# Kernel optimization log

Measured on AMD Instinct MI355X. Metric: run time of the kernel, lower is better.

## Reference

```python
import jax, jax.numpy as jnp
import numpy as np

EPS = 1e-5  # BatchNorm eps; BN applied in eval mode with running_mean=0, running_var=1


def conv1x1(x, w, b=None):
    # x: [B,C,H,W], w: [O,C] -> [B,O,H,W]
    y = jnp.einsum('bchw,oc->bohw', x, w)
    if b is not None:
        y = y + b[None, :, None, None]
    return y


def bn_eval(x, gamma, beta):
    # running_mean=0, running_var=1
    scale = gamma / jnp.sqrt(1.0 + EPS)
    return x * scale[None, :, None, None] + beta[None, :, None, None]


def glnl_forward(x, mask, wt_nl, bt_nl, wp_nl, bp_nl, wt_l, bt_l, wp_l, bp_l,
                 wg_nl, bg_nl, wg_l, bg_l, wW, bW, gW, betaW, wWl, gWl, betaWl):
    B, C, H, W = x.shape
    I = wt_nl.shape[0]
    N = H * W

    # non-local branch score [B,N,N]
    th_nl = conv1x1(x, wt_nl, bt_nl).reshape(B, I, N)
    ph_nl = conv1x1(x, wp_nl, bp_nl).reshape(B, I, N)
    score_nl = jax.nn.softmax(jnp.einsum('bin,bim->bnm', th_nl, ph_nl), axis=-1)

    # local branch: mask-gated projections, score [B,N,N]
    m = mask.reshape(B, 1, N)
    th_l = conv1x1(x, wt_l, bt_l).reshape(B, I, N) * m
    ph_l = conv1x1(x, wp_l, bp_l).reshape(B, I, N) * m
    score_l = jax.nn.softmax(jnp.einsum('bin,bim->bnm', th_l, ph_l), axis=-1)

    # value projections [B,I,N]
    g_nl = conv1x1(x, wg_nl, bg_nl).reshape(B, I, N)
    g_l = conv1x1(x, wg_l, bg_l).reshape(B, I, N)

    # attention aggregation -> [B,I,H,W]
    y_nl = jnp.einsum('bnm,bim->bin', score_nl, g_nl).reshape(B, I, H, W)
    y_l = jnp.einsum('bnm,bim->bin', score_l, g_l).reshape(B, I, H, W)

    # W_local: conv1x1 (no bias) -> ReLU -> BN
    y_l = bn_eval(jax.nn.relu(conv1x1(y_l, wWl)), gWl, betaWl)

    y = y_nl + y_l
    # W: conv1x1 -> ReLU -> BN, then residual
    W_y = bn_eval(jax.nn.relu(conv1x1(y, wW, bW)), gW, betaW)
    return W_y + x


def setup_inputs() -> dict:
    key = jax.random.key(0)
    ks = jax.random.split(key, 20)
    B, C, I, H, W = 4, 128, 64, 64, 64
    s = 0.02
    inp = {
        'x': jax.random.normal(ks[0], (B, C, H, W), jnp.float32),
        'mask': (jax.random.uniform(ks[1], (B, 1, H, W)) > 0.5).astype(jnp.float32),
        'wt_nl': jax.random.normal(ks[2], (I, C)) * s, 'bt_nl': jnp.zeros((I,)),
        'wp_nl': jax.random.normal(ks[3], (I, C)) * s, 'bp_nl': jnp.zeros((I,)),
        'wt_l': jax.random.normal(ks[4], (I, C)) * s, 'bt_l': jnp.zeros((I,)),
        'wp_l': jax.random.normal(ks[5], (I, C)) * s, 'bp_l': jnp.zeros((I,)),
        'wg_nl': jax.random.normal(ks[6], (I, C)) * s, 'bg_nl': jnp.zeros((I,)),
        'wg_l': jax.random.normal(ks[7], (I, C)) * s, 'bg_l': jnp.zeros((I,)),
        'wW': jax.random.normal(ks[8], (C, I)) * s, 'bW': jnp.zeros((C,)),
        'gW': jnp.ones((C,)), 'betaW': jnp.zeros((C,)),
        'wWl': jax.random.normal(ks[9], (I, I)) * s,
        'gWl': jnp.ones((I,)), 'betaWl': jnp.zeros((I,)),
    }
    return inp


def reference(x, mask, wt_nl, bt_nl, wp_nl, bp_nl, wt_l, bt_l, wp_l, bp_l,
              wg_nl, bg_nl, wg_l, bg_l, wW, bW, gW, betaW, wWl, gWl, betaWl):
    return glnl_forward(x, mask, wt_nl, bt_nl, wp_nl, bp_nl, wt_l, bt_l, wp_l, bp_l,
                        wg_nl, bg_nl, wg_l, bg_l, wW, bW, gW, betaW, wWl, gWl, betaWl)
```

## Files before the change

### kernel.cpp

```cpp
#include <hip/hip_runtime.h>

typedef unsigned short u16;
typedef __attribute__((ext_vector_type(8))) short short8;
typedef __attribute__((ext_vector_type(4))) float floatx4;
typedef __attribute__((ext_vector_type(2))) unsigned int uint2e;

#define MFMA16(a, b, c) __builtin_amdgcn_mfma_f32_16x16x32_bf16((a), (b), (c), 0, 0, 0)
#define LOG2E 1.44269504088896340736f

#define SZ_P ((size_t)4 * 64 * 4096)
#define NSP 4

__device__ __forceinline__ float bf2f(u16 u) {
    union { unsigned int i; float f; } v; v.i = ((unsigned int)u) << 16; return v.f;
}
__device__ __forceinline__ u16 f2bf(float f) {
    union { float f; unsigned int i; } v; v.f = f;
    unsigned int r = v.i + 0x7fffu + ((v.i >> 16) & 1u);
    return (u16)(r >> 16);
}
__device__ __forceinline__ unsigned int cvtpk(float a, float b) {
    unsigned int r;
    asm("v_cvt_pk_bf16_f32 %0, %1, %2" : "=v"(r) : "v"(a), "v"(b));
    return r;
}
__device__ __forceinline__ void plswap32(unsigned int &a, unsigned int &b) {
#if __has_builtin(__builtin_amdgcn_permlane32_swap)
    uint2e r = __builtin_amdgcn_permlane32_swap(a, b, false, false);
    a = r.x; b = r.y;
#else
    asm volatile("v_permlane32_swap_b32 %0, %1" : "+v"(a), "+v"(b));
#endif
}
__device__ __forceinline__ void plswap16(unsigned int &a, unsigned int &b) {
#if __has_builtin(__builtin_amdgcn_permlane16_swap)
    uint2e r = __builtin_amdgcn_permlane16_swap(a, b, false, false);
    a = r.x; b = r.y;
#else
    asm volatile("v_permlane16_swap_b32 %0, %1" : "+v"(a), "+v"(b));
#endif
}
__device__ __forceinline__ int swz(int row, int g) {
    return row * 64 + (((g ^ (row & 7)) << 3));
}
__device__ __forceinline__ void gload16(const void* g, void* l) {
    __builtin_amdgcn_global_load_lds(
        (const __attribute__((address_space(1))) unsigned char*)g,
        (__attribute__((address_space(3))) unsigned char*)l, 16, 0, 0);
}

__global__ __launch_bounds__(256) void k_prep_w(
    const float* __restrict__ w0, const float* __restrict__ w1,
    const float* __restrict__ w2, const float* __restrict__ w3,
    const float* __restrict__ w4, const float* __restrict__ w5,
    const float* __restrict__ wWl, const float* __restrict__ wW,
    u16* __restrict__ wbf)
{
    const int idx = blockIdx.x * 256 + threadIdx.x;
    float v;
    if (idx < 49152) {
        const int j = idx >> 13, off = idx & 8191;
        const float* s = (j == 0) ? w0 : (j == 1) ? w1 : (j == 2) ? w2
                       : (j == 3) ? w3 : (j == 4) ? w4 : w5;
        v = s[off];
    } else if (idx < 53248) {
        v = wWl[idx - 49152];
    } else {
        v = wW[idx - 53248];
    }
    wbf[idx] = f2bf(v);
}

__global__ __launch_bounds__(256) void k_proj(
    const float* __restrict__ x, const float* __restrict__ mask,
    const u16* __restrict__ wbf,
    const float* __restrict__ bq0f, const float* __restrict__ bk0f,
    const float* __restrict__ bv0f,
    const float* __restrict__ bq1f, const float* __restrict__ bk1f,
    const float* __restrict__ bv1f,
    u16* __restrict__ q0, u16* __restrict__ k0, u16* __restrict__ v0,
    u16* __restrict__ q1, u16* __restrict__ k1, u16* __restrict__ v1)
{
    __shared__ __align__(16) u16 xt_s[64 * 136];
    const int n0 = blockIdx.x * 64, b = blockIdx.y;

    const int t = threadIdx.x, w = t >> 6, lane = t & 63;
    const int quad = lane >> 4, l15 = lane & 15;
    const float* xb = x + ((size_t)b << 19);

    for (int idx = t; idx < 8192; idx += 256) {
        const int c = idx >> 6, n = idx & 63;
        xt_s[n * 136 + c] = f2bf(xb[((size_t)c << 12) + n0 + n]);
    }
    __syncthreads();

    short8 ax[4];
#pragma unroll
    for (int cc = 0; cc < 4; ++cc)
        ax[cc] = *(const short8*)&xt_s[(w * 16 + l15) * 136 + quad * 8 + cc * 32];

#pragma unroll
    for (int br = 0; br < 2; ++br) {
        const u16* wq = wbf + br * 24576;
        const u16* wk = wq + 8192;
        const u16* wv = wk + 8192;
        const float* bq = br ? bq1f : bq0f;
        const float* bk = br ? bk1f : bk0f;
        const float* bv = br ? bv1f : bv0f;
        u16* q = br ? q1 : q0;  u16* k = br ? k1 : k0;  u16* v = br ? v1 : v0;

        float mv[4] = {1.f, 1.f, 1.f, 1.f};
        if (br) {
#pragma unroll
            for (int r = 0; r < 4; ++r)
                mv[r] = mask[((size_t)b << 12) + n0 + w * 16 + quad * 4 + r];
        }

#pragma unroll
        for (int qk = 0; qk < 2; ++qk) {
            const u16* wsel = qk ? wk : wq;
            const float* bb = qk ? bk : bq;
            u16* o = qk ? k : q;
            const float qscale = qk ? 1.0f : LOG2E;
#pragma unroll
            for (int ns = 0; ns < 4; ++ns) {
                floatx4 acc = {0.f, 0.f, 0.f, 0.f};
                const u16* wp = wsel + (ns * 16 + l15) * 128 + quad * 8;
#pragma unroll
                for (int cc = 0; cc < 4; ++cc)
                    acc = MFMA16(ax[cc], *(const short8*)(wp + cc * 32), acc);
                const float bias_i = bb[ns * 16 + l15];
#pragma unroll
                for (int r = 0; r < 4; ++r) {
                    const float val = (acc[r] + bias_i) * mv[r] * qscale;
                    o[((size_t)b << 18) + (size_t)(n0 + w * 16 + quad * 4 + r) * 64
                      + ns * 16 + l15] = f2bf(val);
                }
            }
        }

        short8 aw[4];
#pragma unroll
        for (int cc = 0; cc < 4; ++cc)
            aw[cc] = *(const short8*)(wv + (w * 16 + l15) * 128 + quad * 8 + cc * 32);
        float bvr[4];
#pragma unroll
        for (int r = 0; r < 4; ++r) bvr[r] = bv[w * 16 + quad * 4 + r];
#pragma unroll
        for (int ns = 0; ns < 4; ++ns) {
            floatx4 acc = {0.f, 0.f, 0.f, 0.f};
#pragma unroll
            for (int cc = 0; cc < 4; ++cc)
                acc = MFMA16(aw[cc],
                    *(const short8*)&xt_s[(ns * 16 + l15) * 136 + quad * 8 + cc * 32], acc);
#pragma unroll
            for (int r = 0; r < 4; ++r) {
                v[((size_t)b << 18) + ((size_t)(w * 16 + quad * 4 + r) << 12)
                  + n0 + ns * 16 + l15] = f2bf(acc[r] + bvr[r]);
            }
        }
    }
}

__global__ __launch_bounds__(512, 4) void k_flash(
    const u16* __restrict__ Q0, const u16* __restrict__ K0,
    const u16* __restrict__ V0,
    const u16* __restrict__ Q1, const u16* __restrict__ K1,
    const u16* __restrict__ V1,
    u16* __restrict__ num, float* __restrict__ den)
{
    constexpr int NIT = 4096 / NSP / 64;

    __shared__ __align__(16) u16 smem[18432];

    const int flat = blockIdx.x;
    const int g = flat & 31, tile = flat >> 5;
    const int b = g >> 3, br = (g >> 2) & 1, sp = g & 3;
    const int z = br * NSP + sp;
    const int qb = tile * 256;
    const size_t base = ((size_t)b << 18);
    const u16* Q = (br ? Q1 : Q0) + base;
    const u16* K = (br ? K1 : K0) + base;
    const u16* V = (br ? V1 : V0) + base;
    u16* numo = num + (size_t)z * SZ_P + base;
    float* deno = den + z * 16384 + b * 4096;

    const int t = threadIdx.x, w = t >> 6, lane = t & 63;
    const int quad = lane >> 4, l15 = lane & 15;
    const int pw = w * 32 * 72;

    const int r0 = t >> 3;
    const int gx = (t & 7) ^ ((t >> 3) & 7);
    const u16* Kp0 = K + (size_t)r0 * 64 + gx * 8;
    const u16* Vp0 = V + ((size_t)r0 << 12) + gx * 8;
    u16* kw = smem + w * 512;
    u16* vw = smem + 8192 + w * 512;

    short8 aq[2][2];
#pragma unroll
    for (int t2 = 0; t2 < 2; ++t2)
#pragma unroll
        for (int s = 0; s < 2; ++s)
            aq[t2][s] = *(const short8*)(Q + (size_t)(qb + w * 32 + t2 * 16 + l15) * 64
                                         + s * 32 + quad * 8);

    floatx4 oacc[4][2];
#pragma unroll
    for (int it = 0; it < 4; ++it)
#pragma unroll
        for (int t2 = 0; t2 < 2; ++t2) oacc[it][t2] = (floatx4){0.f, 0.f, 0.f, 0.f};
    floatx4 dacc4[2];
    dacc4[0] = (floatx4){0.f, 0.f, 0.f, 0.f};
    dacc4[1] = (floatx4){0.f, 0.f, 0.f, 0.f};
    const short8 vone = {(short)0x3F80, (short)0x3F80, (short)0x3F80, (short)0x3F80,
                         (short)0x3F80, (short)0x3F80, (short)0x3F80, (short)0x3F80};

    const int roff = tile & (NIT - 1);
    const int m_beg = sp * (4096 / NSP);

    {
        const int m0 = m_beg + (roff << 6);
        gload16(Kp0 + (size_t)m0 * 64, kw);
        gload16(Vp0 + m0, vw);
    }

    for (int j = 0; j < NIT; ++j) {
        const int cur = j & 1;
        asm volatile("s_waitcnt vmcnt(0)" ::: "memory");
        __builtin_amdgcn_sched_barrier(0);
        __syncthreads();
        if (j + 1 < NIT) {
            const int mn = m_beg + (((roff + j + 1) & (NIT - 1)) << 6);
            gload16(Kp0 + (size_t)mn * 64, kw + (cur ^ 1) * 4096);
            gload16(Vp0 + mn, vw + (cur ^ 1) * 4096);
        }
        const u16* kt = smem + cur * 4096;
        const u16* vt = smem + 8192 + cur * 4096;

#pragma unroll
        for (int s = 0; s < 2; ++s) {
            unsigned int w0[2][2], w1[2][2];
#pragma unroll
            for (int mtl = 0; mtl < 2; ++mtl) {
                const int mt = s * 2 + mtl;
                const int ko = swz(mt * 16 + l15, quad);
                const short8 ka0 = *(const short8*)(kt + ko);
                const short8 ka1 = *(const short8*)(kt + (ko ^ 32));
#pragma unroll
                for (int t2 = 0; t2 < 2; ++t2) {
                    floatx4 acc = {0.f, 0.f, 0.f, 0.f};
                    __builtin_amdgcn_s_setprio(1);
                    acc = MFMA16(ka0, aq[t2][0], acc);
                    acc = MFMA16(ka1, aq[t2][1], acc);
                    __builtin_amdgcn_s_setprio(0);
                    const float e0 = __builtin_amdgcn_exp2f(acc[0]);
                    const float e1 = __builtin_amdgcn_exp2f(acc[1]);
                    const float e2 = __builtin_amdgcn_exp2f(acc[2]);
                    const float e3 = __builtin_amdgcn_exp2f(acc[3]);
                    w0[mtl][t2] = cvtpk(e0, e1);
                    w1[mtl][t2] = cvtpk(e2, e3);
                }
            }
            short8 pb[2];
#pragma unroll
            for (int t2 = 0; t2 < 2; ++t2) {
                unsigned int a0 = w0[0][t2], b0 = w0[1][t2];
                unsigned int a1 = w1[0][t2], b1 = w1[1][t2];
                plswap32(a0, b0); plswap16(a0, b0);
                plswap32(a1, b1); plswap16(a1, b1);
                union { unsigned int u[4]; short8 s8; } cv;
                cv.u[0] = a0; cv.u[1] = a1; cv.u[2] = b0; cv.u[3] = b1;
                pb[t2] = cv.s8;
            }
            __builtin_amdgcn_s_setprio(1);
#pragma unroll
            for (int it = 0; it < 4; ++it) {
                const short8 va = *(const short8*)(vt + swz(it * 16 + l15, s * 4 + quad));
#pragma unroll
                for (int t2 = 0; t2 < 2; ++t2)
                    oacc[it][t2] = MFMA16(va, pb[t2], oacc[it][t2]);
            }
            dacc4[0] = MFMA16(vone, pb[0], dacc4[0]);
            dacc4[1] = MFMA16(vone, pb[1], dacc4[1]);
            __builtin_amdgcn_s_setprio(0);
        }
    }

    if (quad == 0) {
#pragma unroll
        for (int t2 = 0; t2 < 2; ++t2)
            deno[qb + w * 32 + t2 * 16 + l15] = dacc4[t2][0];
    }

    __syncthreads();
#pragma unroll
    for (int it = 0; it < 4; ++it)
#pragma unroll
        for (int t2 = 0; t2 < 2; ++t2) {
            *(uint2*)&smem[pw + (t2 * 16 + l15) * 72 + it * 16 + quad * 4] =
                make_uint2(cvtpk(oacc[it][t2][0], oacc[it][t2][1]),
                           cvtpk(oacc[it][t2][2], oacc[it][t2][3]));
        }
    __syncthreads();
#pragma unroll
    for (int ch = t; ch < 2048; ch += 512) {
        const int row = ch >> 3, cg = ch & 7;
        *(short8*)(numo + (size_t)(qb + row) * 64 + cg * 8) =
            *(const short8*)&smem[(row >> 5) * 2304 + (row & 31) * 72 + cg * 8];
    }
}

__global__ __launch_bounds__(256) void k_epi(
    const u16* __restrict__ num, const float* __restrict__ den,
    const u16* __restrict__ wbf,
    const float* __restrict__ gWl, const float* __restrict__ betaWl,
    const float* __restrict__ bW, const float* __restrict__ gW,
    const float* __restrict__ betaW,
    const float* __restrict__ x, float* __restrict__ out)
{
    __shared__ __align__(16) u16 yl_s[32 * 72];
    __shared__ __align__(16) u16 ynl_s[32 * 72];
    __shared__ __align__(16) u16 yy_s[32 * 72];
    const int b = blockIdx.y, n0 = blockIdx.x * 32;
    const int t = threadIdx.x, w = t >> 6, lane = t & 63;
    const int quad = lane >> 4, l15 = lane & 15;
    const size_t ybase = ((size_t)b << 18) + (size_t)n0 * 64;

    {
        const int row = t >> 3, cg = t & 7;
        float dn = 0.f, dl = 0.f;
#pragma unroll
        for (int sp = 0; sp < NSP; ++sp) {
            dn += den[sp * 16384 + b * 4096 + n0 + row];
            dl += den[(NSP + sp) * 16384 + b * 4096 + n0 + row];
        }
        const float inl = 1.0f / dn, ilo = 1.0f / dl;
        float an[8] = {0, 0, 0, 0, 0, 0, 0, 0}, al[8] = {0, 0, 0, 0, 0, 0, 0, 0};
#pragma unroll
        for (int sp = 0; sp < NSP; ++sp) {
            const short8 vn = *(const short8*)(num + (size_t)sp * SZ_P + ybase + row * 64 + cg * 8);
            const short8 vl = *(const short8*)(num + (size_t)(NSP + sp) * SZ_P + ybase + row * 64 + cg * 8);
#pragma unroll
            for (int j = 0; j < 8; ++j) {
                an[j] += bf2f((u16)vn[j]);
                al[j] += bf2f((u16)vl[j]);
            }
        }
        short8 ynl8, yl8;
#pragma unroll
        for (int j = 0; j < 8; ++j) {
            ynl8[j] = (short)f2bf(an[j] * inl);
            yl8[j]  = (short)f2bf(al[j] * ilo);
        }
        *(short8*)&ynl_s[row * 72 + cg * 8] = ynl8;
        *(short8*)&yl_s[row * 72 + cg * 8] = yl8;
    }
    __syncthreads();
    const float rsq = rsqrtf(1.0f + 1e-5f);
    const u16* wblW = wbf + 49152;
    const u16* wbW  = wbf + 53248;

    {
        const short8 a0 = *(const short8*)(wblW + (w * 16 + l15) * 64 + quad * 8);
        const short8 a1 = *(const short8*)(wblW + (w * 16 + l15) * 64 + 32 + quad * 8);
        float sc[4], bt[4];
#pragma unroll
        for (int r = 0; r < 4; ++r) {
            const int io = w * 16 + quad * 4 + r;
            sc[r] = gWl[io] * rsq;
            bt[r] = betaWl[io];
        }
#pragma unroll
        for (int nh = 0; nh < 2; ++nh) {
            floatx4 acc = {0.f, 0.f, 0.f, 0.f};
            const u16* bp_ = &yl_s[(nh * 16 + l15) * 72 + quad * 8];
            acc = MFMA16(a0, *(const short8*)bp_, acc);
            acc = MFMA16(a1, *(const short8*)(bp_ + 32), acc);
#pragma unroll
            for (int r = 0; r < 4; ++r) {
                const int io = w * 16 + quad * 4 + r;
                float val = fmaxf(acc[r], 0.f) * sc[r] + bt[r];
                val += bf2f(ynl_s[(nh * 16 + l15) * 72 + io]);
                yy_s[(nh * 16 + l15) * 72 + io] = f2bf(val);
            }
        }
    }
    __syncthreads();

#pragma unroll
    for (int rb = 0; rb < 2; ++rb) {
        const int c0 = rb * 64 + w * 16;
        const short8 a0 = *(const short8*)(wbW + (c0 + l15) * 64 + quad * 8);
        const short8 a1 = *(const short8*)(wbW + (c0 + l15) * 64 + 32 + quad * 8);
        float bs[4], sc[4], bt[4];
#pragma unroll
        for (int r = 0; r < 4; ++r) {
            const int c = c0 + quad * 4 + r;
            bs[r] = bW[c];
            sc[r] = gW[c] * rsq;
            bt[r] = betaW[c];
        }
#pragma unroll
        for (int nh = 0; nh < 2; ++nh) {
            floatx4 acc = {0.f, 0.f, 0.f, 0.f};
            const u16* bp_ = &yy_s[(nh * 16 + l15) * 72 + quad * 8];
            acc = MFMA16(a0, *(const short8*)bp_, acc);
            acc = MFMA16(a1, *(const short8*)(bp_ + 32), acc);
#pragma unroll
            for (int r = 0; r < 4; ++r) {
                const int c = c0 + quad * 4 + r;
                float val = fmaxf(acc[r] + bs[r], 0.f) * sc[r] + bt[r];
                const size_t xi = ((size_t)b << 19) + ((size_t)c << 12) + n0 + nh * 16 + l15;
                out[xi] = val + x[xi];
            }
        }
    }
}

extern "C" void kernel_launch(void* const* d_in, const int* in_sizes, int n_in,
                              void* d_out, int out_size, void* d_ws, size_t ws_size,
                              hipStream_t stream) {
    const float* x      = (const float*)d_in[0];
    const float* mask   = (const float*)d_in[1];
    const float* wt_nl  = (const float*)d_in[2];  const float* bt_nl = (const float*)d_in[3];
    const float* wp_nl  = (const float*)d_in[4];  const float* bp_nl = (const float*)d_in[5];
    const float* wt_l   = (const float*)d_in[6];  const float* bt_l  = (const float*)d_in[7];
    const float* wp_l   = (const float*)d_in[8];  const float* bp_l  = (const float*)d_in[9];
    const float* wg_nl  = (const float*)d_in[10]; const float* bg_nl = (const float*)d_in[11];
    const float* wg_l   = (const float*)d_in[12]; const float* bg_l  = (const float*)d_in[13];
    const float* wW     = (const float*)d_in[14]; const float* bW    = (const float*)d_in[15];
    const float* gW     = (const float*)d_in[16]; const float* betaW = (const float*)d_in[17];
    const float* wWl    = (const float*)d_in[18]; const float* gWl   = (const float*)d_in[19];
    const float* betaWl = (const float*)d_in[20];

    u16* ws  = (u16*)d_ws;
    u16* wbf = ws;
    u16* q0  = wbf + 61440;
    u16* k0  = q0 + SZ_P;
    u16* v0  = k0 + SZ_P;
    u16* q1  = v0 + SZ_P;
    u16* k1  = q1 + SZ_P;
    u16* v1  = k1 + SZ_P;
    u16* num = v1 + SZ_P;
    float* den = (float*)(num + (size_t)2 * NSP * SZ_P);

    k_prep_w<<<dim3(240), 256, 0, stream>>>(wt_nl, wp_nl, wg_nl,
                                            wt_l, wp_l, wg_l, wWl, wW, wbf);
    k_proj<<<dim3(64, 4), 256, 0, stream>>>(x, mask, wbf,
        bt_nl, bp_nl, bg_nl, bt_l, bp_l, bg_l,
        q0, k0, v0, q1, k1, v1);
    k_flash<<<dim3(512), 512, 0, stream>>>(q0, k0, v0, q1, k1, v1, num, den);
    k_epi<<<dim3(128, 4), 256, 0, stream>>>(num, den, wbf, gWl, betaWl,
                                            bW, gW, betaW, x, (float*)d_out);
}
```

Measured before the change: 166.3 us.

## Fuse epilogue into flash kernel via last-arriving-block election

Result: slower. 358.4 us (+115.5%).

```diff
diff --git a/kernel.cpp b/kernel.cpp
--- a/kernel.cpp
+++ b/kernel.cpp
@@ -54,9 +54,10 @@
     const float* __restrict__ w2, const float* __restrict__ w3,
     const float* __restrict__ w4, const float* __restrict__ w5,
     const float* __restrict__ wWl, const float* __restrict__ wW,
-    u16* __restrict__ wbf)
+    u16* __restrict__ wbf, int* __restrict__ ctr)
 {
     const int idx = blockIdx.x * 256 + threadIdx.x;
+    if (blockIdx.x == 0 && threadIdx.x < 64) ctr[threadIdx.x] = 0;
     float v;
     if (idx < 49152) {
         const int j = idx >> 13, off = idx & 8191;
@@ -87,10 +88,15 @@
     const int t = threadIdx.x, w = t >> 6, lane = t & 63;
     const int quad = lane >> 4, l15 = lane & 15;
     const float* xb = x + ((size_t)b << 19);
-
-    for (int idx = t; idx < 8192; idx += 256) {
-        const int c = idx >> 6, n = idx & 63;
-        xt_s[n * 136 + c] = f2bf(xb[((size_t)c << 12) + n0 + n]);
+    const float4* xb4 = (const float4*)xb;
+
+    for (int idx = t; idx < 2048; idx += 256) {
+        const int c = idx >> 4, n4 = (idx & 15) * 4;
+        const float4 v4 = xb4[((size_t)c << 10) + (n0 >> 2) + (idx & 15)];
+        xt_s[(n4 + 0) * 136 + c] = f2bf(v4.x);
+        xt_s[(n4 + 1) * 136 + c] = f2bf(v4.y);
+        xt_s[(n4 + 2) * 136 + c] = f2bf(v4.z);
+        xt_s[(n4 + 3) * 136 + c] = f2bf(v4.w);
     }
     __syncthreads();
 
@@ -167,11 +173,17 @@
     const u16* __restrict__ V0,
     const u16* __restrict__ Q1, const u16* __restrict__ K1,
     const u16* __restrict__ V1,
-    u16* __restrict__ num, float* __restrict__ den)
+    u16* __restrict__ num, float* __restrict__ den,
+    const u16* __restrict__ wbf, int* __restrict__ ctr,
+    const float* __restrict__ gWl, const float* __restrict__ betaWl,
+    const float* __restrict__ bW, const float* __restrict__ gW,
+    const float* __restrict__ betaW,
+    const float* __restrict__ x, float* __restrict__ out)
 {
     constexpr int NIT = 4096 / NSP / 64;
 
     __shared__ __align__(16) u16 smem[18432];
+    __shared__ int elect_s;
 
     const int flat = blockIdx.x;
     const int g = flat & 31, tile = flat >> 5;
@@ -308,112 +320,116 @@
         *(short8*)(numo + (size_t)(qb + row) * 64 + cg * 8) =
             *(const short8*)&smem[(row >> 5) * 2304 + (row & 31) * 72 + cg * 8];
     }
-}
-
-__global__ __launch_bounds__(256) void k_epi(
-    const u16* __restrict__ num, const float* __restrict__ den,
-    const u16* __restrict__ wbf,
-    const float* __restrict__ gWl, const float* __restrict__ betaWl,
-    const float* __restrict__ bW, const float* __restrict__ gW,
-    const float* __restrict__ betaW,
-    const float* __restrict__ x, float* __restrict__ out)
-{
-    __shared__ __align__(16) u16 yl_s[32 * 72];
-    __shared__ __align__(16) u16 ynl_s[32 * 72];
-    __shared__ __align__(16) u16 yy_s[32 * 72];
-    const int b = blockIdx.y, n0 = blockIdx.x * 32;
-    const int t = threadIdx.x, w = t >> 6, lane = t & 63;
-    const int quad = lane >> 4, l15 = lane & 15;
-    const size_t ybase = ((size_t)b << 18) + (size_t)n0 * 64;
-
-    {
-        const int row = t >> 3, cg = t & 7;
-        float dn = 0.f, dl = 0.f;
-#pragma unroll
-        for (int sp = 0; sp < NSP; ++sp) {
-            dn += den[sp * 16384 + b * 4096 + n0 + row];
-            dl += den[(NSP + sp) * 16384 + b * 4096 + n0 + row];
-        }
-        const float inl = 1.0f / dn, ilo = 1.0f / dl;
-        float an[8] = {0, 0, 0, 0, 0, 0, 0, 0}, al[8] = {0, 0, 0, 0, 0, 0, 0, 0};
-#pragma unroll
-        for (int sp = 0; sp < NSP; ++sp) {
-            const short8 vn = *(const short8*)(num + (size_t)sp * SZ_P + ybase + row * 64 + cg * 8);
-            const short8 vl = *(const short8*)(num + (size_t)(NSP + sp) * SZ_P + ybase + row * 64 + cg * 8);
-#pragma unroll
-            for (int j = 0; j < 8; ++j) {
-                an[j] += bf2f((u16)vn[j]);
-                al[j] += bf2f((u16)vl[j]);
-            }
-        }
-        short8 ynl8, yl8;
-#pragma unroll
-        for (int j = 0; j < 8; ++j) {
-            ynl8[j] = (short)f2bf(an[j] * inl);
-            yl8[j]  = (short)f2bf(al[j] * ilo);
-        }
-        *(short8*)&ynl_s[row * 72 + cg * 8] = ynl8;
-        *(short8*)&yl_s[row * 72 + cg * 8] = yl8;
-    }
+
+    __threadfence();
     __syncthreads();
+    if (t == 0) {
+        const int old = atomicAdd(&ctr[b * 16 + tile], 1);
+        elect_s = (old == 7);
+    }
+    __syncthreads();
+    if (!elect_s) return;
+    __threadfence();
+
+    const int half = w >> 2, wl = w & 3, tl = t & 255;
+    u16* yl_sE  = smem + half * 6912;
+    u16* ynl_sE = yl_sE + 2304;
+    u16* yy_sE  = yl_sE + 4608;
     const float rsq = rsqrtf(1.0f + 1e-5f);
     const u16* wblW = wbf + 49152;
     const u16* wbW  = wbf + 53248;
 
-    {
-        const short8 a0 = *(const short8*)(wblW + (w * 16 + l15) * 64 + quad * 8);
-        const short8 a1 = *(const short8*)(wblW + (w * 16 + l15) * 64 + 32 + quad * 8);
-        float sc[4], bt[4];
-#pragma unroll
-        for (int r = 0; r < 4; ++r) {
-            const int io = w * 16 + quad * 4 + r;
-            sc[r] = gWl[io] * rsq;
-            bt[r] = betaWl[io];
-        }
-#pragma unroll
-        for (int nh = 0; nh < 2; ++nh) {
-            floatx4 acc = {0.f, 0.f, 0.f, 0.f};
-            const u16* bp_ = &yl_s[(nh * 16 + l15) * 72 + quad * 8];
-            acc = MFMA16(a0, *(const short8*)bp_, acc);
-            acc = MFMA16(a1, *(const short8*)(bp_ + 32), acc);
+    for (int nh8 = 0; nh8 < 4; ++nh8) {
+        const int n0e = qb + (nh8 * 2 + half) * 32;
+        const size_t ybase = base + (size_t)n0e * 64;
+
+        {
+            const int row = tl >> 3, cg = tl & 7;
+            float dn = 0.f, dl = 0.f;
+#pragma unroll
+            for (int sp2 = 0; sp2 < NSP; ++sp2) {
+                dn += den[sp2 * 16384 + b * 4096 + n0e + row];
+                dl += den[(NSP + sp2) * 16384 + b * 4096 + n0e + row];
+            }
+            const float inl = 1.0f / dn, ilo = 1.0f / dl;
+            float an[8] = {0, 0, 0, 0, 0, 0, 0, 0}, al[8] = {0, 0, 0, 0, 0, 0, 0, 0};
+#pragma unroll
+            for (int sp2 = 0; sp2 < NSP; ++sp2) {
+                const short8 vn = *(const short8*)(num + (size_t)sp2 * SZ_P + ybase + row * 64 + cg * 8);
+                const short8 vl = *(const short8*)(num + (size_t)(NSP + sp2) * SZ_P + ybase + row * 64 + cg * 8);
+#pragma unroll
+                for (int jj = 0; jj < 8; ++jj) {
+                    an[jj] += bf2f((u16)vn[jj]);
+                    al[jj] += bf2f((u16)vl[jj]);
+                }
+            }
+            short8 ynl8, yl8;
+#pragma unroll
+            for (int jj = 0; jj < 8; ++jj) {
+                ynl8[jj] = (short)f2bf(an[jj] * inl);
+                yl8[jj]  = (short)f2bf(al[jj] * ilo);
+            }
+            *(short8*)&ynl_sE[row * 72 + cg * 8] = ynl8;
+            *(short8*)&yl_sE[row * 72 + cg * 8] = yl8;
+        }
+        __syncthreads();
+
+        {
+            const short8 a0 = *(const short8*)(wblW + (wl * 16 + l15) * 64 + quad * 8);
+            const short8 a1 = *(const short8*)(wblW + (wl * 16 + l15) * 64 + 32 + quad * 8);
+            float sc[4], bt[4];
 #pragma unroll
             for (int r = 0; r < 4; ++r) {
-                const int io = w * 16 + quad * 4 + r;
-                float val = fmaxf(acc[r], 0.f) * sc[r] + bt[r];
-                val += bf2f(ynl_s[(nh * 16 + l15) * 72 + io]);
-                yy_s[(nh * 16 + l15) * 72 + io] = f2bf(val);
-            }
-        }
-    }
-    __syncthreads();
-
-#pragma unroll
-    for (int rb = 0; rb < 2; ++rb) {
-        const int c0 = rb * 64 + w * 16;
-        const short8 a0 = *(const short8*)(wbW + (c0 + l15) * 64 + quad * 8);
-        const short8 a1 = *(const short8*)(wbW + (c0 + l15) * 64 + 32 + quad * 8);
-        float bs[4], sc[4], bt[4];
-#pragma unroll
-        for (int r = 0; r < 4; ++r) {
-            const int c = c0 + quad * 4 + r;
-            bs[r] = bW[c];
-            sc[r] = gW[c] * rsq;
-            bt[r] = betaW[c];
-        }
-#pragma unroll
-        for (int nh = 0; nh < 2; ++nh) {
-            floatx4 acc = {0.f, 0.f, 0.f, 0.f};
-            const u16* bp_ = &yy_s[(nh * 16 + l15) * 72 + quad * 8];
-            acc = MFMA16(a0, *(const short8*)bp_, acc);
-            acc = MFMA16(a1, *(const short8*)(bp_ + 32), acc);
+                const int io = wl * 16 + quad * 4 + r;
+                sc[r] = gWl[io] * rsq;
+                bt[r] = betaWl[io];
+            }
+#pragma unroll
+            for (int nh = 0; nh < 2; ++nh) {
+                floatx4 acc = {0.f, 0.f, 0.f, 0.f};
+                const u16* bp_ = &yl_sE[(nh * 16 + l15) * 72 + quad * 8];
+                acc = MFMA16(a0, *(const short8*)bp_, acc);
+                acc = MFMA16(a1, *(const short8*)(bp_ + 32), acc);
+#pragma unroll
+                for (int r = 0; r < 4; ++r) {
+                    const int io = wl * 16 + quad * 4 + r;
+                    float val = fmaxf(acc[r], 0.f) * sc[r] + bt[r];
+                    val += bf2f(ynl_sE[(nh * 16 + l15) * 72 + io]);
+                    yy_sE[(nh * 16 + l15) * 72 + io] = f2bf(val);
+                }
+            }
+        }
+        __syncthreads();
+
+#pragma unroll
+        for (int rb = 0; rb < 2; ++rb) {
+            const int c0 = rb * 64 + wl * 16;
+            const short8 a0 = *(const short8*)(wbW + (c0 + l15) * 64 + quad * 8);
+            const short8 a1 = *(const short8*)(wbW + (c0 + l15) * 64 + 32 + quad * 8);
+            float bs[4], sc[4], bt[4];
 #pragma unroll
             for (int r = 0; r < 4; ++r) {
                 const int c = c0 + quad * 4 + r;
-                float val = fmaxf(acc[r] + bs[r], 0.f) * sc[r] + bt[r];
-                const size_t xi = ((size_t)b << 19) + ((size_t)c << 12) + n0 + nh * 16 + l15;
-                out[xi] = val + x[xi];
-            }
-        }
+                bs[r] = bW[c];
+                sc[r] = gW[c] * rsq;
+                bt[r] = betaW[c];
+            }
+#pragma unroll
+            for (int nh = 0; nh < 2; ++nh) {
+                floatx4 acc = {0.f, 0.f, 0.f, 0.f};
+                const u16* bp_ = &yy_sE[(nh * 16 + l15) * 72 + quad * 8];
+                acc = MFMA16(a0, *(const short8*)bp_, acc);
+                acc = MFMA16(a1, *(const short8*)(bp_ + 32), acc);
+#pragma unroll
+                for (int r = 0; r < 4; ++r) {
+                    const int c = c0 + quad * 4 + r;
+                    float val = fmaxf(acc[r] + bs[r], 0.f) * sc[r] + bt[r];
+                    const size_t xi = ((size_t)b << 19) + ((size_t)c << 12) + n0e + nh * 16 + l15;
+                    out[xi] = val + x[xi];
+                }
+            }
+        }
+        __syncthreads();
     }
 }
 
@@ -443,13 +459,14 @@
     u16* v1  = k1 + SZ_P;
     u16* num = v1 + SZ_P;
     float* den = (float*)(num + (size_t)2 * NSP * SZ_P);
+    int* ctr = (int*)(den + 2 * NSP * 16384);
 
     k_prep_w<<<dim3(240), 256, 0, stream>>>(wt_nl, wp_nl, wg_nl,
-                                            wt_l, wp_l, wg_l, wWl, wW, wbf);
+                                            wt_l, wp_l, wg_l, wWl, wW, wbf, ctr);
     k_proj<<<dim3(64, 4), 256, 0, stream>>>(x, mask, wbf,
         bt_nl, bp_nl, bg_nl, bt_l, bp_l, bg_l,
         q0, k0, v0, q1, k1, v1);
-    k_flash<<<dim3(512), 512, 0, stream>>>(q0, k0, v0, q1, k1, v1, num, den);
-    k_epi<<<dim3(128, 4), 256, 0, stream>>>(num, den, wbf, gWl, betaWl,
-                                            bW, gW, betaW, x, (float*)d_out);
-}
+    k_flash<<<dim3(512), 512, 0, stream>>>(q0, k0, v0, q1, k1, v1, num, den,
+                                           wbf, ctr, gWl, betaWl, bW, gW, betaW,
+                                           x, (float*)d_out);
+}
```
